# Optimization experiments

Measured on AMD Instinct MI355X. Metric: run time of the kernel, lower is better.

## Reference

```python
import jax, jax.numpy as jnp
import numpy as np

N = 50000      # nodes per object type (2 types)
F = 128        # input feature dim (num_feat)
H = 64         # FLAGS.hidden1 == FLAGS.hidden2
E = 800000     # edges per relation
NET = 4        # edge types: (0,0),(0,1),(1,0),(1,1); for k: dst type i=k//2, src type j=k%2


def setup_inputs() -> dict:
    key = jax.random.key(0)
    ks = jax.random.split(key, 7)
    x0 = jax.random.normal(ks[0], (N, F), jnp.float32)
    x1 = jax.random.normal(ks[1], (N, F), jnp.float32)
    src = jax.random.randint(ks[2], (NET, E), 0, N, jnp.int32)
    dst = jax.random.randint(ks[3], (NET, E), 0, N, jnp.int32)
    # normalized adjacency values (~1/avg_degree keeps activations stable)
    ew = jax.random.uniform(ks[4], (NET, E), jnp.float32) / 16.0
    W1 = jax.random.normal(ks[5], (NET, F, H), jnp.float32) / np.sqrt(F).astype(np.float32)
    Wl = jax.random.normal(ks[6], (NET, NET, H, H), jnp.float32) / np.sqrt(H).astype(np.float32)
    return {"x0": x0, "x1": x1, "src": src, "dst": dst, "ew": ew, "W1": W1, "Wl": Wl}


def _spmm(src_k, dst_k, w_k, x):
    # sparse [N_i, N_j] adjacency @ dense x: gather + weighted scatter-add
    return jax.ops.segment_sum(w_k[:, None] * x[src_k], dst_k, num_segments=N)


def _layer(xs, Ws, src, dst, ew, relu):
    # xs: [x_type0, x_type1]; per edge type (i,j): out[i] += A_ij @ (x_j @ W_ij)
    outs = [jnp.zeros((N, Ws.shape[-1]), xs[0].dtype) for _ in range(2)]
    for k in range(NET):
        i, j = k // 2, k % 2
        outs[i] = outs[i] + _spmm(src[k], dst[k], ew[k], xs[j] @ Ws[k])
    if relu:
        outs = [jax.nn.relu(o) for o in outs]
    return outs


def reference(x0, x1, src, dst, ew, W1, Wl):
    h1 = _layer([x0, x1], W1, src, dst, ew, relu=True)       # hidden1
    e1 = _layer(h1, Wl[0], src, dst, ew, relu=True)          # embeddings1
    e2 = _layer(e1, Wl[1], src, dst, ew, relu=True)          # embeddings2
    e3 = _layer(e2, Wl[2], src, dst, ew, relu=True)          # embeddings3
    emb = _layer(e3, Wl[3], src, dst, ew, relu=False)        # embeddings = add_n(reltyp4), no relu
    # final concat per object type: [hidden1, embeddings1, embeddings] -> (N, 3H)
    return jnp.stack([jnp.concatenate([h1[t], e1[t], emb[t]], axis=1) for t in range(2)])
```

## Files before the change

kernel.cpp:

```cpp
#include <hip/hip_runtime.h>
#include <cstddef>

#define NREL 4
#define NSUP 2
#define HD 64
#define FD 128
#define BSHIFT 8
#define BUCKET 256
#define CHUNK 16384

static inline int idiv_up(int a, int b) { return (a + b - 1) / b; }

typedef __attribute__((ext_vector_type(8))) short bf16x8;
typedef __attribute__((ext_vector_type(4))) float f32x4;

__device__ __forceinline__ unsigned short f2bf(float f) {
    unsigned int u = __float_as_uint(f);
    unsigned int r = (u + 0x7FFFu + ((u >> 16) & 1u)) >> 16;
    return (unsigned short)r;
}
__device__ __forceinline__ float bflo(unsigned int v) {
    return __uint_as_float(v << 16);
}
__device__ __forceinline__ float bfhi(unsigned int v) {
    return __uint_as_float(v & 0xFFFF0000u);
}
__device__ __forceinline__ unsigned int cvtpk_bf16(float lo, float hi) {
    unsigned int r;
    asm("v_cvt_pk_bf16_f32 %0, %1, %2" : "=v"(r) : "v"(lo), "v"(hi));
    return r;
}


__global__ void bhist_kernel(const int* __restrict__ dst, int* __restrict__ bhist,
                             int E2, int NBP) {
    int k = blockIdx.y;
    extern __shared__ int lh[];
    for (int i = threadIdx.x; i < NBP; i += blockDim.x) lh[i] = 0;
    __syncthreads();
    const int* dk = dst + (size_t)k * E2;
    for (int e = blockIdx.x * blockDim.x + threadIdx.x; e < E2; e += gridDim.x * blockDim.x)
        atomicAdd(&lh[dk[e] >> BSHIFT], 1);
    __syncthreads();
    int* bh = bhist + (size_t)k * NBP;
    for (int i = threadIdx.x; i < NBP; i += blockDim.x)
        if (lh[i]) atomicAdd(&bh[i], lh[i]);
}


__global__ void bscan_kernel(const int* __restrict__ bhist, int* __restrict__ bptr,
                             int* __restrict__ gcur, int NBP, int E2) {
    int k = blockIdx.x;
    __shared__ int wsum[16];
    int tid = threadIdx.x, wid = tid >> 6, lane = tid & 63;
    int v = (tid < NBP) ? bhist[(size_t)k * NBP + tid] : 0;
    int x = v;
    #pragma unroll
    for (int off = 1; off < 64; off <<= 1) {
        int y = __shfl_up(x, off, 64);
        if (lane >= off) x += y;
    }
    if (lane == 63) wsum[wid] = x;
    __syncthreads();
    if (wid == 0) {
        int s = (lane < 16) ? wsum[lane] : 0;
        #pragma unroll
        for (int off = 1; off < 16; off <<= 1) {
            int y = __shfl_up(s, off, 64);
            if (lane >= off) s += y;
        }
        if (lane < 16) wsum[lane] = s;
    }
    __syncthreads();
    int excl = x - v + (wid ? wsum[wid - 1] : 0);
    if (tid < NBP) {
        bptr[(size_t)k * (NBP + 1) + tid] = excl;
        gcur[(size_t)k * NBP + tid] = excl;
    }
    if (tid == 0) bptr[(size_t)k * (NBP + 1) + NBP] = E2;
}


__global__ void part_kernel(const int* __restrict__ src, const int* __restrict__ dst,
                            const float* __restrict__ ew, int* __restrict__ gcur,
                            int2* __restrict__ staged, int E, int E2, int N, int NBP) {
    int k = blockIdx.y;
    extern __shared__ int sh[];
    int* lcnt = sh;
    int* lbase = sh + NBP;
    for (int i = threadIdx.x; i < NBP; i += blockDim.x) lcnt[i] = 0;
    __syncthreads();
    const int* sk = src + (size_t)k * E2;
    const int* dk = dst + (size_t)k * E2;
    const float* wk = ew + (size_t)k * E2;
    int base = blockIdx.x * CHUNK;
    int n = min(CHUNK, E2 - base);
    for (int i = threadIdx.x; i < n; i += blockDim.x)
        atomicAdd(&lcnt[dk[base + i] >> BSHIFT], 1);
    __syncthreads();
    for (int i = threadIdx.x; i < NBP; i += blockDim.x) {
        int c = lcnt[i];
        lbase[i] = c ? atomicAdd(&gcur[(size_t)k * NBP + i], c) : 0;
    }
    __syncthreads();
    for (int i = threadIdx.x; i < NBP; i += blockDim.x) lcnt[i] = 0;
    __syncthreads();
    int2* out = staged + (size_t)k * E2;
    for (int i = threadIdx.x; i < n; i += blockDim.x) {
        int gi = base + i;
        int d = dk[gi];
        int b = d >> BSHIFT;
        int row = sk[gi] + ((gi >= E) ? N : 0);
        int local = atomicAdd(&lcnt[b], 1);
        out[lbase[b] + local] =
            make_int2(row | ((d & (BUCKET - 1)) << 17), __float_as_int(wk[gi]));
    }
}


__global__ void bsort_kernel(const int2* __restrict__ staged, const int* __restrict__ bptr,
                             int* __restrict__ rowptr, unsigned int* __restrict__ edges,
                             int E2, int N, int NBP) {
    int k = blockIdx.y;
    int b = blockIdx.x;
    __shared__ int hist[BUCKET];
    __shared__ int excl[BUCKET];
    __shared__ int cur[BUCKET];
    __shared__ int wsum2[4];
    int tid = threadIdx.x;
    int wid = tid >> 6, lane = tid & 63;
    if (tid < BUCKET) hist[tid] = 0;
    __syncthreads();
    int beg = bptr[(size_t)k * (NBP + 1) + b];
    int end = bptr[(size_t)k * (NBP + 1) + b + 1];
    const int2* in = staged + (size_t)k * E2;
    for (int i = beg + tid; i < end; i += blockDim.x)
        atomicAdd(&hist[(in[i].x >> 17) & (BUCKET - 1)], 1);
    __syncthreads();
    int v = 0, x = 0;
    if (tid < BUCKET) {
        v = hist[tid];
        x = v;
        #pragma unroll
        for (int off = 1; off < 64; off <<= 1) {
            int y = __shfl_up(x, off, 64);
            if (lane >= off) x += y;
        }
        if (lane == 63) wsum2[wid] = x;
    }
    __syncthreads();
    if (tid == 0) {
        int s = 0;
        #pragma unroll
        for (int j = 0; j < 4; ++j) { int t = wsum2[j]; wsum2[j] = s; s += t; }
    }
    __syncthreads();
    if (tid < BUCKET) {
        int e = x - v + wsum2[wid];
        excl[tid] = e;
        cur[tid] = e;
    }
    __syncthreads();
    unsigned int* outp = edges + (size_t)k * E2;
    for (int i = beg + tid; i < end; i += blockDim.x) {
        int2 q = in[i];
        int dl = (q.x >> 17) & (BUCKET - 1);
        int pos = atomicAdd(&cur[dl], 1);
        unsigned int wb = (unsigned int)(f2bf(__int_as_float(q.y)) & 0x7FFF);
        outp[beg + pos] = ((unsigned int)q.x & 0x1FFFFu) | (wb << 17);
    }
    int node0 = b * BUCKET;
    if (tid < BUCKET && node0 + tid < N)
        rowptr[(size_t)k * (N + 1) + node0 + tid] = beg + excl[tid];
    if (b == 0 && tid == 0) rowptr[(size_t)k * (N + 1) + N] = E2;
}


__global__ void convw_kernel(const float* __restrict__ W, unsigned short* __restrict__ Wf,
                             int mats, int KK) {
    int tid = blockIdx.x * blockDim.x + threadIdx.x;
    int total = mats * KK * 4 * 64;
    if (tid >= total) return;
    int l = tid & 63;
    int n = (tid >> 6) & 3;
    int rest = tid >> 8;
    int kk = rest % KK;
    int mat = rest / KK;
    int h = l >> 4, c = l & 15;
    int K = KK * 32;
    const float* Wm = W + (size_t)mat * K * 64;
    unsigned short* o = Wf + (size_t)tid * 8;
    #pragma unroll
    for (int i = 0; i < 8; ++i)
        o[i] = f2bf(Wm[(size_t)(kk * 32 + h * 8 + i) * 64 + n * 16 + c]);
}


template <int K>
__global__ void gemm_mfma_kernel(const unsigned short* __restrict__ Xb,
                                 const unsigned short* __restrict__ Wf,
                                 unsigned short* __restrict__ Ybase, int N) {
    constexpr int KK = K / 32;
    int rel = blockIdx.y;
    const unsigned short* X = Xb + (size_t)(rel & 1) * N * K;
    const bf16x8* Wv = reinterpret_cast<const bf16x8*>(Wf + (size_t)rel * KK * 4 * 64 * 8);
    unsigned short* Y = Ybase + (size_t)rel * N * HD;
    int tid = threadIdx.x;
    int w = tid >> 6, l = tid & 63;
    int lr = l & 15, lh = l >> 4;
    int row0 = blockIdx.x * 128 + w * 32;
    f32x4 acc00 = {0.f,0.f,0.f,0.f}, acc01 = {0.f,0.f,0.f,0.f};
    f32x4 acc02 = {0.f,0.f,0.f,0.f}, acc03 = {0.f,0.f,0.f,0.f};
    f32x4 acc10 = {0.f,0.f,0.f,0.f}, acc11 = {0.f,0.f,0.f,0.f};
    f32x4 acc12 = {0.f,0.f,0.f,0.f}, acc13 = {0.f,0.f,0.f,0.f};
    int r0 = min(row0 + lr, N - 1);
    int r1 = min(row0 + 16 + lr, N - 1);
    const unsigned short* xp0 = X + (size_t)r0 * K + lh * 8;
    const unsigned short* xp1 = X + (size_t)r1 * K + lh * 8;
    #pragma unroll
    for (int kk = 0; kk < KK; ++kk) {
        bf16x8 a0 = *reinterpret_cast<const bf16x8*>(xp0 + kk * 32);
        bf16x8 a1 = *reinterpret_cast<const bf16x8*>(xp1 + kk * 32);
        bf16x8 b0 = Wv[(kk * 4 + 0) * 64 + l];
        bf16x8 b1 = Wv[(kk * 4 + 1) * 64 + l];
        bf16x8 b2 = Wv[(kk * 4 + 2) * 64 + l];
        bf16x8 b3 = Wv[(kk * 4 + 3) * 64 + l];
        acc00 = __builtin_amdgcn_mfma_f32_16x16x32_bf16(a0, b0, acc00, 0, 0, 0);
        acc01 = __builtin_amdgcn_mfma_f32_16x16x32_bf16(a0, b1, acc01, 0, 0, 0);
        acc02 = __builtin_amdgcn_mfma_f32_16x16x32_bf16(a0, b2, acc02, 0, 0, 0);
        acc03 = __builtin_amdgcn_mfma_f32_16x16x32_bf16(a0, b3, acc03, 0, 0, 0);
        acc10 = __builtin_amdgcn_mfma_f32_16x16x32_bf16(a1, b0, acc10, 0, 0, 0);
        acc11 = __builtin_amdgcn_mfma_f32_16x16x32_bf16(a1, b1, acc11, 0, 0, 0);
        acc12 = __builtin_amdgcn_mfma_f32_16x16x32_bf16(a1, b2, acc12, 0, 0, 0);
        acc13 = __builtin_amdgcn_mfma_f32_16x16x32_bf16(a1, b3, acc13, 0, 0, 0);
    }
    #pragma unroll
    for (int reg = 0; reg < 4; ++reg) {
        int rowa = row0 + lh * 4 + reg;
        if (rowa < N) {
            unsigned short* yp = Y + (size_t)rowa * HD + lr;
            yp[0]  = f2bf(acc00[reg]);
            yp[16] = f2bf(acc01[reg]);
            yp[32] = f2bf(acc02[reg]);
            yp[48] = f2bf(acc03[reg]);
        }
        int rowb = row0 + 16 + lh * 4 + reg;
        if (rowb < N) {
            unsigned short* yp = Y + (size_t)rowb * HD + lr;
            yp[0]  = f2bf(acc10[reg]);
            yp[16] = f2bf(acc11[reg]);
            yp[32] = f2bf(acc12[reg]);
            yp[48] = f2bf(acc13[reg]);
        }
    }
}


__global__ void gemm_mfma_f32in_kernel(const float* __restrict__ X0,
                                       const float* __restrict__ X1,
                                       const unsigned short* __restrict__ Wf,
                                       unsigned short* __restrict__ Ybase, int N) {
    constexpr int K = FD;
    constexpr int KK = K / 32;
    int rel = blockIdx.y;
    const float* X = (rel & 1) ? X1 : X0;
    const bf16x8* Wv = reinterpret_cast<const bf16x8*>(Wf + (size_t)rel * KK * 4 * 64 * 8);
    unsigned short* Y = Ybase + (size_t)rel * N * HD;
    int tid = threadIdx.x;
    int w = tid >> 6, l = tid & 63;
    int lr = l & 15, lh = l >> 4;
    int row0 = blockIdx.x * 128 + w * 32;
    f32x4 acc00 = {0.f,0.f,0.f,0.f}, acc01 = {0.f,0.f,0.f,0.f};
    f32x4 acc02 = {0.f,0.f,0.f,0.f}, acc03 = {0.f,0.f,0.f,0.f};
    f32x4 acc10 = {0.f,0.f,0.f,0.f}, acc11 = {0.f,0.f,0.f,0.f};
    f32x4 acc12 = {0.f,0.f,0.f,0.f}, acc13 = {0.f,0.f,0.f,0.f};
    int r0 = min(row0 + lr, N - 1);
    int r1 = min(row0 + 16 + lr, N - 1);
    const float* xp0 = X + (size_t)r0 * K + lh * 8;
    const float* xp1 = X + (size_t)r1 * K + lh * 8;
    #pragma unroll
    for (int kk = 0; kk < KK; ++kk) {
        float4 xa0 = *reinterpret_cast<const float4*>(xp0 + kk * 32);
        float4 xa1 = *reinterpret_cast<const float4*>(xp0 + kk * 32 + 4);
        float4 xb0 = *reinterpret_cast<const float4*>(xp1 + kk * 32);
        float4 xb1 = *reinterpret_cast<const float4*>(xp1 + kk * 32 + 4);
        union { unsigned int u[4]; bf16x8 v; } ca, cb;
        ca.u[0] = cvtpk_bf16(xa0.x, xa0.y);
        ca.u[1] = cvtpk_bf16(xa0.z, xa0.w);
        ca.u[2] = cvtpk_bf16(xa1.x, xa1.y);
        ca.u[3] = cvtpk_bf16(xa1.z, xa1.w);
        cb.u[0] = cvtpk_bf16(xb0.x, xb0.y);
        cb.u[1] = cvtpk_bf16(xb0.z, xb0.w);
        cb.u[2] = cvtpk_bf16(xb1.x, xb1.y);
        cb.u[3] = cvtpk_bf16(xb1.z, xb1.w);
        bf16x8 a0 = ca.v;
        bf16x8 a1 = cb.v;
        bf16x8 b0 = Wv[(kk * 4 + 0) * 64 + l];
        bf16x8 b1 = Wv[(kk * 4 + 1) * 64 + l];
        bf16x8 b2 = Wv[(kk * 4 + 2) * 64 + l];
        bf16x8 b3 = Wv[(kk * 4 + 3) * 64 + l];
        acc00 = __builtin_amdgcn_mfma_f32_16x16x32_bf16(a0, b0, acc00, 0, 0, 0);
        acc01 = __builtin_amdgcn_mfma_f32_16x16x32_bf16(a0, b1, acc01, 0, 0, 0);
        acc02 = __builtin_amdgcn_mfma_f32_16x16x32_bf16(a0, b2, acc02, 0, 0, 0);
        acc03 = __builtin_amdgcn_mfma_f32_16x16x32_bf16(a0, b3, acc03, 0, 0, 0);
        acc10 = __builtin_amdgcn_mfma_f32_16x16x32_bf16(a1, b0, acc10, 0, 0, 0);
        acc11 = __builtin_amdgcn_mfma_f32_16x16x32_bf16(a1, b1, acc11, 0, 0, 0);
        acc12 = __builtin_amdgcn_mfma_f32_16x16x32_bf16(a1, b2, acc12, 0, 0, 0);
        acc13 = __builtin_amdgcn_mfma_f32_16x16x32_bf16(a1, b3, acc13, 0, 0, 0);
    }
    #pragma unroll
    for (int reg = 0; reg < 4; ++reg) {
        int rowa = row0 + lh * 4 + reg;
        if (rowa < N) {
            unsigned short* yp = Y + (size_t)rowa * HD + lr;
            yp[0]  = f2bf(acc00[reg]);
            yp[16] = f2bf(acc01[reg]);
            yp[32] = f2bf(acc02[reg]);
            yp[48] = f2bf(acc03[reg]);
        }
        int rowb = row0 + 16 + lh * 4 + reg;
        if (rowb < N) {
            unsigned short* yp = Y + (size_t)rowb * HD + lr;
            yp[0]  = f2bf(acc10[reg]);
            yp[16] = f2bf(acc11[reg]);
            yp[32] = f2bf(acc12[reg]);
            yp[48] = f2bf(acc13[reg]);
        }
    }
}


__global__ void spmm_kernel(const unsigned short* __restrict__ Ybase,
                            const int* __restrict__ rowptr, const unsigned int* __restrict__ edges,
                            unsigned short* __restrict__ act, float* __restrict__ outp,
                            int N, int E2, int relu) {
    int id = blockIdx.x;
    int g = id & 7;
    int t = g >> 2;
    int pbi = (id >> 3) * 4 + (g & 3);
    int wave = threadIdx.x >> 6;
    int lane = threadIdx.x & 63;
    int d = pbi * 4 + wave;
    if (d >= N) return;
    int h = lane >> 4;
    int c4 = (lane & 15) * 4;
    const unsigned short* Y = Ybase + (size_t)(2 * t) * N * HD;
    const unsigned int* ep = edges + (size_t)t * E2;
    int beg = rowptr[(size_t)t * (N + 1) + d];
    int end = rowptr[(size_t)t * (N + 1) + d + 1];
    float4 a[4];
    #pragma unroll
    for (int j = 0; j < 4; ++j) a[j] = make_float4(0.f, 0.f, 0.f, 0.f);
    if (beg < end) {
        int endm1 = end - 1;
        unsigned int m[8];
        #pragma unroll
        for (int j = 0; j < 8; ++j) {
            int idx = beg + 4 * j + h;
            m[j] = ep[idx < end ? idx : endm1];
        }
        for (int base = beg; ; ) {
            int nb = base + 32;
            bool more = nb < end;
            unsigned int n[8];
            if (more) {
                #pragma unroll
                for (int j = 0; j < 8; ++j) {
                    int idx = nb + 4 * j + h;
                    n[j] = ep[idx < end ? idx : endm1];
                }
            }
            uint2 y[8];
            #pragma unroll
            for (int j = 0; j < 8; ++j)
                y[j] = *reinterpret_cast<const uint2*>(Y + ((m[j] & 0x1FFFFu) * HD + c4));
            #pragma unroll
            for (int j = 0; j < 8; ++j) {
                float w = ((base + 4 * j + h) < end)
                              ? __uint_as_float((m[j] >> 17) << 16) : 0.f;
                a[j & 3].x += w * bflo(y[j].x);
                a[j & 3].y += w * bfhi(y[j].x);
                a[j & 3].z += w * bflo(y[j].y);
                a[j & 3].w += w * bfhi(y[j].y);
            }
            if (!more) break;
            base = nb;
            #pragma unroll
            for (int j = 0; j < 8; ++j) m[j] = n[j];
        }
    }
    float4 s;
    s.x = (a[0].x + a[1].x) + (a[2].x + a[3].x);
    s.y = (a[0].y + a[1].y) + (a[2].y + a[3].y);
    s.z = (a[0].z + a[1].z) + (a[2].z + a[3].z);
    s.w = (a[0].w + a[1].w) + (a[2].w + a[3].w);
    s.x += __shfl_xor(s.x, 16, 64);  s.x += __shfl_xor(s.x, 32, 64);
    s.y += __shfl_xor(s.y, 16, 64);  s.y += __shfl_xor(s.y, 32, 64);
    s.z += __shfl_xor(s.z, 16, 64);  s.z += __shfl_xor(s.z, 32, 64);
    s.w += __shfl_xor(s.w, 16, 64);  s.w += __shfl_xor(s.w, 32, 64);
    if (relu) {
        s.x = fmaxf(s.x, 0.f); s.y = fmaxf(s.y, 0.f);
        s.z = fmaxf(s.z, 0.f); s.w = fmaxf(s.w, 0.f);
    }
    if (lane < 16) {
        if (act) {
            ushort4 ob;
            ob.x = f2bf(s.x); ob.y = f2bf(s.y); ob.z = f2bf(s.z); ob.w = f2bf(s.w);
            *reinterpret_cast<ushort4*>(&act[((size_t)t * N + d) * HD + c4]) = ob;
        }
        if (outp) *reinterpret_cast<float4*>(&outp[((size_t)t * N + d) * 192 + c4]) = s;
    }
}


extern "C" void kernel_launch(void* const* d_in, const int* in_sizes, int n_in,
                              void* d_out, int out_size, void* d_ws, size_t ws_size,
                              hipStream_t stream) {
    const float* x0 = (const float*)d_in[0];
    const float* x1 = (const float*)d_in[1];
    const int* src = (const int*)d_in[2];
    const int* dst = (const int*)d_in[3];
    const float* ew = (const float*)d_in[4];
    const float* W1 = (const float*)d_in[5];
    const float* Wl = (const float*)d_in[6];
    float* out = (float*)d_out;

    int N = in_sizes[0] / FD;
    int E = in_sizes[2] / NREL;
    int E2 = 2 * E;
    int NBP = idiv_up(N, BUCKET);

    char* ws = (char*)d_ws;
    size_t off = 0;
    auto alloc = [&](size_t bytes) -> void* {
        void* p = ws + off;
        off = (off + bytes + 255) & ~(size_t)255;
        return p;
    };
    int* bhist   = (int*)alloc((size_t)NSUP * NBP * 4);
    int* bptr    = (int*)alloc((size_t)NSUP * (NBP + 1) * 4);
    int* gcur    = (int*)alloc((size_t)NSUP * NBP * 4);
    int* rowptr  = (int*)alloc((size_t)NSUP * (N + 1) * 4);
    unsigned int* edges = (unsigned int*)alloc((size_t)NSUP * E2 * 4);
    unsigned short* y    = (unsigned short*)alloc((size_t)NREL * N * HD * 2);
    unsigned short* actb = (unsigned short*)alloc((size_t)2 * N * HD * 2);
    unsigned short* W1f  = (unsigned short*)alloc((size_t)NREL * 4 * 4 * 64 * 8 * 2);
    unsigned short* Wlf  = (unsigned short*)alloc((size_t)16 * 2 * 4 * 64 * 8 * 2);
    int2* staged = (int2*)alloc((size_t)NSUP * E2 * 8);
    (void)ws_size;

    convw_kernel<<<idiv_up(NREL * 4 * 4 * 64, 256), 256, 0, stream>>>(W1, W1f, NREL, 4);
    convw_kernel<<<idiv_up(16 * 2 * 4 * 64, 256), 256, 0, stream>>>(Wl, Wlf, 16, 2);

    hipMemsetAsync(bhist, 0, (size_t)NSUP * NBP * 4, stream);
    bhist_kernel<<<dim3(384, NSUP), 256, NBP * 4, stream>>>(dst, bhist, E2, NBP);
    bscan_kernel<<<NSUP, 1024, 0, stream>>>(bhist, bptr, gcur, NBP, E2);
    part_kernel<<<dim3(idiv_up(E2, CHUNK), NSUP), 1024, 2 * NBP * 4, stream>>>(
        src, dst, ew, gcur, staged, E, E2, N, NBP);
    bsort_kernel<<<dim3(NBP, NSUP), 1024, 0, stream>>>(staged, bptr, rowptr, edges, E2, N, NBP);

    dim3 ggrid(idiv_up(N, 128), NREL);
    int NB4 = idiv_up(N, 4);
    int sgx = idiv_up(NB4, 4) * 8;

    gemm_mfma_f32in_kernel<<<ggrid, 256, 0, stream>>>(x0, x1, W1f, y, N);
    spmm_kernel<<<sgx, 256, 0, stream>>>(y, rowptr, edges, actb, out + 0, N, E2, 1);

    for (int l = 0; l < 4; ++l) {
        gemm_mfma_kernel<HD><<<ggrid, 256, 0, stream>>>(
            actb, Wlf + (size_t)l * 4 * 2 * 4 * 64 * 8, y, N);
        float* op = (l == 0) ? (out + 64) : (l == 3) ? (out + 128) : nullptr;
        unsigned short* ap = (l == 3) ? nullptr : actb;
        int relu = (l == 3) ? 0 : 1;
        spmm_kernel<<<sgx, 256, 0, stream>>>(y, rowptr, edges, ap, op, N, E2, relu);
    }
}
```

Baseline: 451.0 us.

## Replace atomic bucket partition with per-chunk count/scan/place and halve spmm batch

The edge bucketing preprocessing now writes per-chunk bucket histograms, runs a column-wise scan over chunks, and places edges at precomputed offsets. This replaces the global histogram, the memset, the atomic cursor reservation and the recount pass inside the partition kernel. The spmm inner loop now gathers 16 edges per iteration instead of 32, with explicit scalar registers. That lowers register pressure to allow more waves in flight, but leaves fewer gathers outstanding per wave.

```diff
diff --git a/kernel.cpp b/kernel.cpp
--- a/kernel.cpp
+++ b/kernel.cpp
@@ -32,29 +32,40 @@
 }
 
 
-__global__ void bhist_kernel(const int* __restrict__ dst, int* __restrict__ bhist,
-                             int E2, int NBP) {
+__global__ void pcount_kernel(const int* __restrict__ dst, int* __restrict__ ccnt,
+                              int E2, int NBP, int NCH) {
     int k = blockIdx.y;
+    int c = blockIdx.x;
     extern __shared__ int lh[];
     for (int i = threadIdx.x; i < NBP; i += blockDim.x) lh[i] = 0;
     __syncthreads();
     const int* dk = dst + (size_t)k * E2;
-    for (int e = blockIdx.x * blockDim.x + threadIdx.x; e < E2; e += gridDim.x * blockDim.x)
-        atomicAdd(&lh[dk[e] >> BSHIFT], 1);
-    __syncthreads();
-    int* bh = bhist + (size_t)k * NBP;
-    for (int i = threadIdx.x; i < NBP; i += blockDim.x)
-        if (lh[i]) atomicAdd(&bh[i], lh[i]);
-}
-
-
-__global__ void bscan_kernel(const int* __restrict__ bhist, int* __restrict__ bptr,
-                             int* __restrict__ gcur, int NBP, int E2) {
+    int base = c * CHUNK;
+    int n = min(CHUNK, E2 - base);
+    for (int i = threadIdx.x; i < n; i += blockDim.x)
+        atomicAdd(&lh[dk[base + i] >> BSHIFT], 1);
+    __syncthreads();
+    int* out = ccnt + ((size_t)k * NCH + c) * NBP;
+    for (int i = threadIdx.x; i < NBP; i += blockDim.x) out[i] = lh[i];
+}
+
+
+__global__ void pscan_kernel(int* __restrict__ ccnt, int* __restrict__ bptr,
+                             int NBP, int NCH, int E2) {
     int k = blockIdx.x;
-    __shared__ int wsum[16];
-    int tid = threadIdx.x, wid = tid >> 6, lane = tid & 63;
-    int v = (tid < NBP) ? bhist[(size_t)k * NBP + tid] : 0;
-    int x = v;
+    int tid = threadIdx.x;
+    int* cc = ccnt + (size_t)k * NCH * NBP;
+    int total = 0;
+    if (tid < NBP) {
+        for (int c = 0; c < NCH; ++c) {
+            int v = cc[c * NBP + tid];
+            cc[c * NBP + tid] = total;
+            total += v;
+        }
+    }
+    __shared__ int wsum[4];
+    int wid = tid >> 6, lane = tid & 63;
+    int x = total;
     #pragma unroll
     for (int off = 1; off < 64; off <<= 1) {
         int y = __shfl_up(x, off, 64);
@@ -62,49 +73,38 @@
     }
     if (lane == 63) wsum[wid] = x;
     __syncthreads();
-    if (wid == 0) {
-        int s = (lane < 16) ? wsum[lane] : 0;
+    if (tid == 0) {
+        int s = 0;
         #pragma unroll
-        for (int off = 1; off < 16; off <<= 1) {
-            int y = __shfl_up(s, off, 64);
-            if (lane >= off) s += y;
-        }
-        if (lane < 16) wsum[lane] = s;
-    }
-    __syncthreads();
-    int excl = x - v + (wid ? wsum[wid - 1] : 0);
-    if (tid < NBP) {
-        bptr[(size_t)k * (NBP + 1) + tid] = excl;
-        gcur[(size_t)k * NBP + tid] = excl;
-    }
+        for (int j = 0; j < 4; ++j) { int t = wsum[j]; wsum[j] = s; s += t; }
+    }
+    __syncthreads();
+    int excl = x - total + wsum[wid];
+    if (tid < NBP) bptr[(size_t)k * (NBP + 1) + tid] = excl;
     if (tid == 0) bptr[(size_t)k * (NBP + 1) + NBP] = E2;
 }
 
 
-__global__ void part_kernel(const int* __restrict__ src, const int* __restrict__ dst,
-                            const float* __restrict__ ew, int* __restrict__ gcur,
-                            int2* __restrict__ staged, int E, int E2, int N, int NBP) {
+__global__ void pplace_kernel(const int* __restrict__ src, const int* __restrict__ dst,
+                              const float* __restrict__ ew, const int* __restrict__ ccnt,
+                              const int* __restrict__ bptr, int2* __restrict__ staged,
+                              int E, int E2, int N, int NBP, int NCH) {
     int k = blockIdx.y;
+    int c = blockIdx.x;
     extern __shared__ int sh[];
     int* lcnt = sh;
     int* lbase = sh + NBP;
-    for (int i = threadIdx.x; i < NBP; i += blockDim.x) lcnt[i] = 0;
+    const int* cc = ccnt + ((size_t)k * NCH + c) * NBP;
+    for (int i = threadIdx.x; i < NBP; i += blockDim.x) {
+        lbase[i] = bptr[(size_t)k * (NBP + 1) + i] + cc[i];
+        lcnt[i] = 0;
+    }
     __syncthreads();
     const int* sk = src + (size_t)k * E2;
     const int* dk = dst + (size_t)k * E2;
     const float* wk = ew + (size_t)k * E2;
-    int base = blockIdx.x * CHUNK;
+    int base = c * CHUNK;
     int n = min(CHUNK, E2 - base);
-    for (int i = threadIdx.x; i < n; i += blockDim.x)
-        atomicAdd(&lcnt[dk[base + i] >> BSHIFT], 1);
-    __syncthreads();
-    for (int i = threadIdx.x; i < NBP; i += blockDim.x) {
-        int c = lcnt[i];
-        lbase[i] = c ? atomicAdd(&gcur[(size_t)k * NBP + i], c) : 0;
-    }
-    __syncthreads();
-    for (int i = threadIdx.x; i < NBP; i += blockDim.x) lcnt[i] = 0;
-    __syncthreads();
     int2* out = staged + (size_t)k * E2;
     for (int i = threadIdx.x; i < n; i += blockDim.x) {
         int gi = base + i;
@@ -348,52 +348,55 @@
     const unsigned int* ep = edges + (size_t)t * E2;
     int beg = rowptr[(size_t)t * (N + 1) + d];
     int end = rowptr[(size_t)t * (N + 1) + d + 1];
-    float4 a[4];
-    #pragma unroll
-    for (int j = 0; j < 4; ++j) a[j] = make_float4(0.f, 0.f, 0.f, 0.f);
+    float4 a0 = {0.f,0.f,0.f,0.f}, a1 = {0.f,0.f,0.f,0.f};
+    float4 a2 = {0.f,0.f,0.f,0.f}, a3 = {0.f,0.f,0.f,0.f};
     if (beg < end) {
         int endm1 = end - 1;
-        unsigned int m[8];
-        #pragma unroll
-        for (int j = 0; j < 8; ++j) {
-            int idx = beg + 4 * j + h;
-            m[j] = ep[idx < end ? idx : endm1];
+        unsigned int m0, m1, m2, m3;
+        {
+            int i0 = beg + 0 + h, i1 = beg + 4 + h, i2 = beg + 8 + h, i3 = beg + 12 + h;
+            m0 = ep[i0 < end ? i0 : endm1];
+            m1 = ep[i1 < end ? i1 : endm1];
+            m2 = ep[i2 < end ? i2 : endm1];
+            m3 = ep[i3 < end ? i3 : endm1];
         }
         for (int base = beg; ; ) {
-            int nb = base + 32;
+            int nb = base + 16;
             bool more = nb < end;
-            unsigned int n[8];
+            unsigned int n0, n1, n2, n3;
             if (more) {
-                #pragma unroll
-                for (int j = 0; j < 8; ++j) {
-                    int idx = nb + 4 * j + h;
-                    n[j] = ep[idx < end ? idx : endm1];
-                }
+                int i0 = nb + 0 + h, i1 = nb + 4 + h, i2 = nb + 8 + h, i3 = nb + 12 + h;
+                n0 = ep[i0 < end ? i0 : endm1];
+                n1 = ep[i1 < end ? i1 : endm1];
+                n2 = ep[i2 < end ? i2 : endm1];
+                n3 = ep[i3 < end ? i3 : endm1];
             }
-            uint2 y[8];
-            #pragma unroll
-            for (int j = 0; j < 8; ++j)
-                y[j] = *reinterpret_cast<const uint2*>(Y + ((m[j] & 0x1FFFFu) * HD + c4));
-            #pragma unroll
-            for (int j = 0; j < 8; ++j) {
-                float w = ((base + 4 * j + h) < end)
-                              ? __uint_as_float((m[j] >> 17) << 16) : 0.f;
-                a[j & 3].x += w * bflo(y[j].x);
-                a[j & 3].y += w * bfhi(y[j].x);
-                a[j & 3].z += w * bflo(y[j].y);
-                a[j & 3].w += w * bfhi(y[j].y);
-            }
+            uint2 y0 = *reinterpret_cast<const uint2*>(Y + ((m0 & 0x1FFFFu) * HD + c4));
+            uint2 y1 = *reinterpret_cast<const uint2*>(Y + ((m1 & 0x1FFFFu) * HD + c4));
+            uint2 y2 = *reinterpret_cast<const uint2*>(Y + ((m2 & 0x1FFFFu) * HD + c4));
+            uint2 y3 = *reinterpret_cast<const uint2*>(Y + ((m3 & 0x1FFFFu) * HD + c4));
+            float w0 = ((base + 0 + h) < end) ? __uint_as_float((m0 >> 17) << 16) : 0.f;
+            float w1 = ((base + 4 + h) < end) ? __uint_as_float((m1 >> 17) << 16) : 0.f;
+            float w2 = ((base + 8 + h) < end) ? __uint_as_float((m2 >> 17) << 16) : 0.f;
+            float w3 = ((base + 12 + h) < end) ? __uint_as_float((m3 >> 17) << 16) : 0.f;
+            a0.x += w0 * bflo(y0.x); a0.y += w0 * bfhi(y0.x);
+            a0.z += w0 * bflo(y0.y); a0.w += w0 * bfhi(y0.y);
+            a1.x += w1 * bflo(y1.x); a1.y += w1 * bfhi(y1.x);
+            a1.z += w1 * bflo(y1.y); a1.w += w1 * bfhi(y1.y);
+            a2.x += w2 * bflo(y2.x); a2.y += w2 * bfhi(y2.x);
+            a2.z += w2 * bflo(y2.y); a2.w += w2 * bfhi(y2.y);
+            a3.x += w3 * bflo(y3.x); a3.y += w3 * bfhi(y3.x);
+            a3.z += w3 * bflo(y3.y); a3.w += w3 * bfhi(y3.y);
             if (!more) break;
             base = nb;
-            #pragma unroll
-            for (int j = 0; j < 8; ++j) m[j] = n[j];
+            m0 = n0; m1 = n1; m2 = n2; m3 = n3;
         }
     }
     float4 s;
-    s.x = (a[0].x + a[1].x) + (a[2].x + a[3].x);
-    s.y = (a[0].y + a[1].y) + (a[2].y + a[3].y);
-    s.z = (a[0].z + a[1].z) + (a[2].z + a[3].z);
-    s.w = (a[0].w + a[1].w) + (a[2].w + a[3].w);
+    s.x = (a0.x + a1.x) + (a2.x + a3.x);
+    s.y = (a0.y + a1.y) + (a2.y + a3.y);
+    s.z = (a0.z + a1.z) + (a2.z + a3.z);
+    s.w = (a0.w + a1.w) + (a2.w + a3.w);
     s.x += __shfl_xor(s.x, 16, 64);  s.x += __shfl_xor(s.x, 32, 64);
     s.y += __shfl_xor(s.y, 16, 64);  s.y += __shfl_xor(s.y, 32, 64);
     s.z += __shfl_xor(s.z, 16, 64);  s.z += __shfl_xor(s.z, 32, 64);
@@ -429,6 +432,7 @@
     int E = in_sizes[2] / NREL;
     int E2 = 2 * E;
     int NBP = idiv_up(N, BUCKET);
+    int NCH = idiv_up(E2, CHUNK);
 
     char* ws = (char*)d_ws;
     size_t off = 0;
@@ -437,9 +441,8 @@
         off = (off + bytes + 255) & ~(size_t)255;
         return p;
     };
-    int* bhist   = (int*)alloc((size_t)NSUP * NBP * 4);
+    int* ccnt    = (int*)alloc((size_t)NSUP * NCH * NBP * 4);
     int* bptr    = (int*)alloc((size_t)NSUP * (NBP + 1) * 4);
-    int* gcur    = (int*)alloc((size_t)NSUP * NBP * 4);
     int* rowptr  = (int*)alloc((size_t)NSUP * (N + 1) * 4);
     unsigned int* edges = (unsigned int*)alloc((size_t)NSUP * E2 * 4);
     unsigned short* y    = (unsigned short*)alloc((size_t)NREL * N * HD * 2);
@@ -452,11 +455,10 @@
     convw_kernel<<<idiv_up(NREL * 4 * 4 * 64, 256), 256, 0, stream>>>(W1, W1f, NREL, 4);
     convw_kernel<<<idiv_up(16 * 2 * 4 * 64, 256), 256, 0, stream>>>(Wl, Wlf, 16, 2);
 
-    hipMemsetAsync(bhist, 0, (size_t)NSUP * NBP * 4, stream);
-    bhist_kernel<<<dim3(384, NSUP), 256, NBP * 4, stream>>>(dst, bhist, E2, NBP);
-    bscan_kernel<<<NSUP, 1024, 0, stream>>>(bhist, bptr, gcur, NBP, E2);
-    part_kernel<<<dim3(idiv_up(E2, CHUNK), NSUP), 1024, 2 * NBP * 4, stream>>>(
-        src, dst, ew, gcur, staged, E, E2, N, NBP);
+    pcount_kernel<<<dim3(NCH, NSUP), 1024, NBP * 4, stream>>>(dst, ccnt, E2, NBP, NCH);
+    pscan_kernel<<<NSUP, 256, 0, stream>>>(ccnt, bptr, NBP, NCH, E2);
+    pplace_kernel<<<dim3(NCH, NSUP), 1024, 2 * NBP * 4, stream>>>(
+        src, dst, ew, ccnt, bptr, staged, E, E2, N, NBP, NCH);
     bsort_kernel<<<dim3(NBP, NSUP), 1024, 0, stream>>>(staged, bptr, rowptr, edges, E2, N, NBP);
 
     dim3 ggrid(idiv_up(N, 128), NREL);
```

Measured after the change: 425.3 us, median of 2. 1.06x faster.
